# Kernel optimization log

Measured on AMD Instinct MI355X. Metric: run time of the kernel, lower is better.

The kernel has to match this reference:

```python
import jax, jax.numpy as jnp
import numpy as np

INPUT_SIZE = 1024
HIDDEN_SIZE = 1024
LN_EPS = 1e-5


def setup_inputs() -> dict:
    key = jax.random.key(0)
    ks = jax.random.split(key, 8)
    bs, n = 4, 2048
    # Xavier-uniform bound for square (in=out) linear layers
    bound = float(np.sqrt(6.0 / (INPUT_SIZE + HIDDEN_SIZE)))
    x = jax.random.normal(ks[0], (bs, n, INPUT_SIZE), dtype=jnp.float32)
    wq = jax.random.uniform(ks[1], (INPUT_SIZE, HIDDEN_SIZE), jnp.float32, -bound, bound)
    wk = jax.random.uniform(ks[2], (INPUT_SIZE, HIDDEN_SIZE), jnp.float32, -bound, bound)
    wv = jax.random.uniform(ks[3], (INPUT_SIZE, HIDDEN_SIZE), jnp.float32, -bound, bound)
    bq = jnp.zeros((HIDDEN_SIZE,), jnp.float32)
    bk = jnp.zeros((HIDDEN_SIZE,), jnp.float32)
    bv = jnp.zeros((HIDDEN_SIZE,), jnp.float32)
    ln_w = jnp.ones((INPUT_SIZE,), jnp.float32)
    ln_b = jnp.zeros((INPUT_SIZE,), jnp.float32)
    return {"x": x, "wq": wq, "bq": bq, "wk": wk, "bk": bk,
            "wv": wv, "bv": bv, "ln_w": ln_w, "ln_b": ln_b}


def _layernorm(x, w, b):
    mu = jnp.mean(x, axis=-1, keepdims=True)
    var = jnp.mean(jnp.square(x - mu), axis=-1, keepdims=True)
    return (x - mu) * jax.lax.rsqrt(var + LN_EPS) * w + b


def reference(x, wq, bq, wk, bk, wv, bv, ln_w, ln_b):
    # x: [b, n, d_in]
    xn = _layernorm(x, ln_w, ln_b)
    q = jnp.einsum('bnd,dh->bnh', xn, wq) + bq
    k = jnp.einsum('bnd,dh->bnh', xn, wk) + bk
    v = jnp.einsum('bnd,dh->bnh', xn, wv) + bv
    scale = 1.0 / np.sqrt(HIDDEN_SIZE)
    att = jnp.einsum('bqh,bkh->bqk', q, k) * scale  # [b, n, n]
    att = jax.nn.softmax(att, axis=-1)
    out = jnp.einsum('bqk,bkh->bqh', att, v)  # [b, n, h]
    return (att, out)
```

## Files before the change

### kernel.cpp

```cpp
#include <hip/hip_runtime.h>
#include <stdint.h>


typedef __attribute__((ext_vector_type(8))) short short8;
typedef __attribute__((ext_vector_type(4))) float floatx4;
typedef __attribute__((ext_vector_type(4))) uint16_t u16x4;

__device__ __forceinline__ uint16_t f2bf(float f) {
    union { float f; uint32_t u; } v; v.f = f;
    uint32_t r = v.u + 0x7fffu + ((v.u >> 16) & 1u);
    return (uint16_t)(r >> 16);
}

typedef const uint32_t __attribute__((address_space(1)))* gas1_t;
typedef uint32_t __attribute__((address_space(3)))* las3_t;
__device__ __forceinline__ void gload_lds16(const uint16_t* g, uint16_t* l) {
    __builtin_amdgcn_global_load_lds((gas1_t)g, (las3_t)l, 16, 0, 0);
}

__device__ __forceinline__ void s_bar()  { asm volatile("s_barrier" ::: "memory"); }
__device__ __forceinline__ void lgkm0()  { asm volatile("s_waitcnt lgkmcnt(0)" ::: "memory"); }
template<int N> __device__ __forceinline__ void vmw() {
    asm volatile("s_waitcnt vmcnt(%0)" :: "n"(N) : "memory");
}


#define RA(MF, MI)                                                        \
    { Af[(MF)][0] = *(const short8*)(LA + aoff + (MI) * 1024 + ksg0);     \
      Af[(MF)][1] = *(const short8*)(LA + aoff + (MI) * 1024 + ksg1); }
#define RB(NI)                                                            \
    { Bf[(NI)][0] = *(const short8*)(LB + boff + (NI) * 1024 + ksg0);     \
      Bf[(NI)][1] = *(const short8*)(LB + boff + (NI) * 1024 + ksg1); }
#define CLUST(MA, MF, NI0)                                                \
    __builtin_amdgcn_s_setprio(1);                                        \
    _Pragma("unroll") for (int mi = 0; mi < 4; ++mi)                      \
    _Pragma("unroll") for (int nn = 0; nn < 2; ++nn)                      \
    _Pragma("unroll") for (int ks = 0; ks < 2; ++ks)                      \
        acc[(MA) + mi][(NI0) + nn] =                                      \
            __builtin_amdgcn_mfma_f32_16x16x32_bf16(                      \
                Af[(MF) + mi][ks], Bf[(NI0) + nn][ks],                    \
                acc[(MA) + mi][(NI0) + nn], 0, 0, 0);                     \
    __builtin_amdgcn_s_setprio(0);
#define CLUST1(NI)                                                        \
    __builtin_amdgcn_s_setprio(1);                                        \
    _Pragma("unroll") for (int mi = 0; mi < 8; ++mi)                      \
    _Pragma("unroll") for (int ks = 0; ks < 2; ++ks)                      \
        acc[mi][(NI)] = __builtin_amdgcn_mfma_f32_16x16x32_bf16(          \
            Af[mi][ks], Bf[(NI)][ks], acc[mi][(NI)], 0, 0, 0);            \
    __builtin_amdgcn_s_setprio(0);

template<int BN, int EPI>
__device__ __forceinline__ void gemm_core(
    const uint16_t* __restrict__ A, const uint16_t* __restrict__ Bt,
    const int K, const int NT, const int m0, const int n0,
    float* __restrict__ Cf, uint16_t* __restrict__ Cb, const int ldc,
    const float* __restrict__ bq, const float* __restrict__ bk,
    const float* __restrict__ bv, const float alpha)
{
    constexpr int ABUF  = 256 * 64;
    constexpr int BP    = BN / 64;
    constexpr int BBUF  = BN * 64;
    constexpr int BUFSZ = ABUF + BBUF;
    constexpr int OPS   = 4 + BP;
    constexpr int NBUF  = (BN == 128) ? 3 : 2;
    constexpr int WAVES_N = (BN == 128) ? 2 : 4;
    constexpr int MIW  = (BN == 128) ? 4 : 8;
    constexpr int NIW  = BN / (16 * WAVES_N);
    constexpr int NFR  = (BN == 256) ? 4 : MIW;
    __shared__ uint16_t sm[NBUF * BUFSZ + 4096];
    uint16_t* const trash = sm + NBUF * BUFSZ;

    const int t = threadIdx.x;

    const int srow = t >> 3;
    const int sseg = (t & 7) ^ (srow & 7);
    const uint16_t* gA = A + (size_t)(m0 + srow) * K + sseg * 8;
    const uint16_t* gB = Bt + (size_t)(n0 + srow) * K + sseg * 8;

    auto STGALL = [&](int kt, int bi) {
        const int live = kt < NT;
        const size_t ko = (size_t)(live ? kt : 0) * 64;
        uint16_t* const db = sm + bi * BUFSZ + t * 8;
        uint16_t* const tr = trash + t * 8;
#pragma unroll
        for (int p = 0; p < 4; ++p)
            gload_lds16(gA + (size_t)(p * 64) * K + ko,
                        live ? (db + p * 4096) : tr);
#pragma unroll
        for (int p = 0; p < BP; ++p)
            gload_lds16(gB + (size_t)(p * 64) * K + ko,
                        live ? (db + ABUF + p * 4096) : tr);
    };

    const int lane = t & 63;
    const int wid  = t >> 6;
    const int wm   = wid / WAVES_N;
    const int wn   = wid % WAVES_N;
    const int quad = lane >> 4;
    const int lrow = lane & 15;
    const int swz  = lrow & 7;
    const int ksg0 = (quad ^ swz) * 8;
    const int ksg1 = ((4 + quad) ^ swz) * 8;
    const int aoff = (wm * (16 * MIW) + lrow) * 64;
    const int boff = (wn * (16 * NIW) + lrow) * 64;

    floatx4 acc[MIW][NIW];
#pragma unroll
    for (int mi = 0; mi < MIW; ++mi)
#pragma unroll
        for (int ni = 0; ni < NIW; ++ni)
            acc[mi][ni] = floatx4{0.f, 0.f, 0.f, 0.f};

    short8 Af[NFR][2];
    short8 Bf[NIW][2];

    STGALL(0, 0);
    STGALL(1, 1);
    vmw<OPS>();
    s_bar();

    int bcur = 0, bstage = 2;
    for (int te = 0; te < NT; ++te) {
        const int bi = (BN == 128) ? bcur : (te & 1);
        const uint16_t* LA = sm + bi * BUFSZ;
        const uint16_t* LB = LA + ABUF;

        if constexpr (BN == 256) {
            RA(0, 0) RA(1, 1) RA(2, 2) RA(3, 3)
            RB(0) RB(1) RB(2) RB(3)
            CLUST(0, 0, 0) CLUST(0, 0, 2)
            RA(0, 4) RA(1, 5) RA(2, 6) RA(3, 7)
            lgkm0(); s_bar();
            STGALL(te + 2, bi);
            CLUST(4, 0, 0) CLUST(4, 0, 2)
            vmw<OPS>(); s_bar();
        } else if constexpr (BN == 192) {
            RA(0, 0) RA(1, 1) RA(2, 2) RA(3, 3)
            RA(4, 4) RA(5, 5) RA(6, 6) RA(7, 7)
            RB(0) RB(1) RB(2)
            CLUST(0, 0, 0) CLUST(4, 4, 0)
            lgkm0(); s_bar();
            STGALL(te + 2, bi);
            CLUST1(2)
            vmw<OPS>(); s_bar();
        } else {
            STGALL(te + 2, bstage);
            RA(0, 0) RA(1, 1) RA(2, 2) RA(3, 3)
            RB(0) RB(1) RB(2) RB(3)
            CLUST(0, 0, 0) CLUST(0, 0, 2)
            lgkm0();
            vmw<OPS>(); s_bar();
            bcur   = (bcur == 2) ? 0 : bcur + 1;
            bstage = (bstage == 2) ? 0 : bstage + 1;
        }
    }

    vmw<0>();

    const int rbase = m0 + wm * (16 * MIW) + quad * 4;
    const int cbase = n0 + wn * (16 * NIW) + lrow;

    if constexpr (EPI == 1) {
        float bc[NIW];
#pragma unroll
        for (int ni = 0; ni < NIW; ++ni) {
            const int col = cbase + ni * 16;
            const int z = col >> 10;
            const float* bp = (z == 0) ? bq : ((z == 1) ? bk : bv);
            bc[ni] = bp[col & 1023];
        }
#pragma unroll
        for (int mi = 0; mi < MIW; ++mi) {
#pragma unroll
            for (int ni = 0; ni < NIW; ++ni) {
                const int row = rbase + mi * 16;
                const int col = cbase + ni * 16;
                const int z = col >> 10, h = col & 1023;
#pragma unroll
                for (int r = 0; r < 4; ++r)
                    Cb[(size_t)z * 8388608 + (size_t)(row + r) * 1024 + h] =
                        f2bf(acc[mi][ni][r] + bc[ni]);
            }
        }
    } else {
#pragma unroll
        for (int mi = 0; mi < MIW; ++mi) {
#pragma unroll
            for (int ni = 0; ni < NIW; ++ni) {
                const int row = rbase + mi * 16;
                const int col = cbase + ni * 16;
#pragma unroll
                for (int r = 0; r < 4; ++r)
                    Cf[(size_t)(row + r) * ldc + col] = acc[mi][ni][r] * alpha;
            }
        }
    }
}

__global__ __launch_bounds__(512, 2) void k_qkv(
    const uint16_t* __restrict__ xn, const uint16_t* __restrict__ wt,
    const float* __restrict__ bq, const float* __restrict__ bk,
    const float* __restrict__ bv, uint16_t* __restrict__ qkv)
{
    const int flat = blockIdx.y * 16 + blockIdx.x;
    const int s = (flat & 7) * 64 + (flat >> 3);
    const int bx = s & 15, by = s >> 4;
    gemm_core<192, 1>(xn, wt, 1024, 16, by * 256, bx * 192,
                      nullptr, qkv, 0, bq, bk, bv, 0.f);
}

__global__ __launch_bounds__(512, 2) void k_scores(
    const uint16_t* __restrict__ q, const uint16_t* __restrict__ k,
    float* __restrict__ S)
{
    const int flat = blockIdx.z * 64 + blockIdx.y * 8 + blockIdx.x;
    const int s = (flat & 7) * 32 + (flat >> 3);
    const int z = s >> 6, y = (s >> 3) & 7, x = s & 7;
    gemm_core<256, 0>(q + (size_t)z * 2048 * 1024, k + (size_t)z * 2048 * 1024,
                      1024, 16, y * 256, x * 256,
                      S + (size_t)z * 2048 * 2048, nullptr, 2048,
                      nullptr, nullptr, nullptr, 0.03125f);
}

__global__ __launch_bounds__(512, 2) void k_out(
    const uint16_t* __restrict__ attb, const uint16_t* __restrict__ vt,
    float* __restrict__ out)
{
    const int flat = blockIdx.z * 64 + blockIdx.y * 8 + blockIdx.x;
    const int s = (flat & 7) * 32 + (flat >> 3);
    const int z = s >> 6, y = (s >> 3) & 7, x = s & 7;
    gemm_core<128, 0>(attb + (size_t)z * 2048 * 2048, vt + (size_t)z * 1024 * 2048,
                      2048, 32, y * 256, x * 128,
                      out + (size_t)z * 2048 * 1024, nullptr, 1024,
                      nullptr, nullptr, nullptr, 1.0f);
}

__global__ __launch_bounds__(256) void k_ln(
    const float* __restrict__ x, const float* __restrict__ lw,
    const float* __restrict__ lb, uint16_t* __restrict__ xn)
{
    const int row = blockIdx.x;
    const int t = threadIdx.x;
    const float* xr = x + (size_t)row * 1024;
    const float4 xv = ((const float4*)xr)[t];
    float s  = xv.x + xv.y + xv.z + xv.w;
    float s2 = xv.x * xv.x + xv.y * xv.y + xv.z * xv.z + xv.w * xv.w;
#pragma unroll
    for (int off = 32; off > 0; off >>= 1) {
        s  += __shfl_xor(s, off);
        s2 += __shfl_xor(s2, off);
    }
    __shared__ float ps[4], ps2[4];
    const int w = t >> 6, lane = t & 63;
    if (lane == 0) { ps[w] = s; ps2[w] = s2; }
    __syncthreads();
    s  = ps[0] + ps[1] + ps[2] + ps[3];
    s2 = ps2[0] + ps2[1] + ps2[2] + ps2[3];
    const float mu  = s * (1.f / 1024.f);
    const float var = s2 * (1.f / 1024.f) - mu * mu;
    const float rs  = rsqrtf(var + 1e-5f);
    const float4 wv = ((const float4*)lw)[t];
    const float4 bv = ((const float4*)lb)[t];
    u16x4 o;
    o.x = f2bf((xv.x - mu) * rs * wv.x + bv.x);
    o.y = f2bf((xv.y - mu) * rs * wv.y + bv.y);
    o.z = f2bf((xv.z - mu) * rs * wv.z + bv.z);
    o.w = f2bf((xv.w - mu) * rs * wv.w + bv.w);
    ((u16x4*)(xn + (size_t)row * 1024))[t] = o;
}

__global__ void k_wt(const float* __restrict__ wq, const float* __restrict__ wk,
                     const float* __restrict__ wv, uint16_t* __restrict__ wt)
{
    __shared__ float tile[32][33];
    const int z = blockIdx.z;
    const float* W = (z == 0) ? wq : ((z == 1) ? wk : wv);
    uint16_t* T = wt + (size_t)z * 1024 * 1024;
    const int c0 = blockIdx.x * 32, r0 = blockIdx.y * 32;
    const int tx = threadIdx.x, ty = threadIdx.y;
#pragma unroll
    for (int i = 0; i < 4; i++)
        tile[ty + 8 * i][tx] = W[(size_t)(r0 + ty + 8 * i) * 1024 + c0 + tx];
    __syncthreads();
#pragma unroll
    for (int i = 0; i < 4; i++)
        T[(size_t)(c0 + ty + 8 * i) * 1024 + r0 + tx] = f2bf(tile[tx][ty + 8 * i]);
}

__global__ __launch_bounds__(256) void k_vt(
    const uint16_t* __restrict__ v, uint16_t* __restrict__ vt)
{
    __shared__ uint16_t tile[64][68];
    const int b = blockIdx.z;
    const uint16_t* V = v + (size_t)b * 2048 * 1024;
    uint16_t* T = vt + (size_t)b * 1024 * 2048;
    const int h0 = blockIdx.x * 64, t0 = blockIdx.y * 64;
    const int t = threadIdx.x;
    const int rr = t >> 4;
    const int cc = (t & 15) * 4;
#pragma unroll
    for (int i = 0; i < 4; i++) {
        const int tok = rr + 16 * i;
        *(u16x4*)&tile[tok][cc] =
            *(const u16x4*)&V[(size_t)(t0 + tok) * 1024 + h0 + cc];
    }
    __syncthreads();
#pragma unroll
    for (int i = 0; i < 4; i++) {
        const int h = rr + 16 * i;
        u16x4 o;
        o.x = tile[cc + 0][h];
        o.y = tile[cc + 1][h];
        o.z = tile[cc + 2][h];
        o.w = tile[cc + 3][h];
        *(u16x4*)&T[(size_t)(h0 + h) * 2048 + t0 + cc] = o;
    }
}

__global__ __launch_bounds__(256) void k_softmax(
    float* __restrict__ S, uint16_t* __restrict__ attb)
{
    const size_t row = blockIdx.x;
    float* p = S + row * 2048;
    const int t = threadIdx.x;
    float4 a = ((float4*)p)[2 * t];
    float4 b = ((float4*)p)[2 * t + 1];
    float m = fmaxf(fmaxf(fmaxf(a.x, a.y), fmaxf(a.z, a.w)),
                    fmaxf(fmaxf(b.x, b.y), fmaxf(b.z, b.w)));
#pragma unroll
    for (int off = 32; off > 0; off >>= 1) m = fmaxf(m, __shfl_xor(m, off));
    __shared__ float pm[4], pl[4];
    const int w = t >> 6, lane = t & 63;
    if (lane == 0) pm[w] = m;
    __syncthreads();
    m = fmaxf(fmaxf(pm[0], pm[1]), fmaxf(pm[2], pm[3]));

    a.x = __expf(a.x - m); a.y = __expf(a.y - m);
    a.z = __expf(a.z - m); a.w = __expf(a.w - m);
    b.x = __expf(b.x - m); b.y = __expf(b.y - m);
    b.z = __expf(b.z - m); b.w = __expf(b.w - m);
    float s = a.x + a.y + a.z + a.w + b.x + b.y + b.z + b.w;
#pragma unroll
    for (int off = 32; off > 0; off >>= 1) s += __shfl_xor(s, off);
    if (lane == 0) pl[w] = s;
    __syncthreads();
    s = pl[0] + pl[1] + pl[2] + pl[3];
    const float inv = 1.f / s;

    a.x *= inv; a.y *= inv; a.z *= inv; a.w *= inv;
    b.x *= inv; b.y *= inv; b.z *= inv; b.w *= inv;
    ((float4*)p)[2 * t]     = a;
    ((float4*)p)[2 * t + 1] = b;

    uint16_t* q = attb + row * 2048 + t * 8;
    u16x4 o0, o1;
    o0.x = f2bf(a.x); o0.y = f2bf(a.y); o0.z = f2bf(a.z); o0.w = f2bf(a.w);
    o1.x = f2bf(b.x); o1.y = f2bf(b.y); o1.z = f2bf(b.z); o1.w = f2bf(b.w);
    ((u16x4*)q)[0] = o0;
    ((u16x4*)q)[1] = o1;
}

extern "C" void kernel_launch(void* const* d_in, const int* in_sizes, int n_in,
                              void* d_out, int out_size, void* d_ws, size_t ws_size,
                              hipStream_t stream)
{
    const float* x  = (const float*)d_in[0];
    const float* wq = (const float*)d_in[1];
    const float* bq = (const float*)d_in[2];
    const float* wk = (const float*)d_in[3];
    const float* bk = (const float*)d_in[4];
    const float* wv = (const float*)d_in[5];
    const float* bv = (const float*)d_in[6];
    const float* lw = (const float*)d_in[7];
    const float* lb = (const float*)d_in[8];

    float* att = (float*)d_out;
    float* out = (float*)d_out + (size_t)16777216;

    uint16_t* xn = (uint16_t*)d_out;
    uint16_t* wt = (uint16_t*)d_out + (size_t)8388608;

    uint16_t* ws   = (uint16_t*)d_ws;
    uint16_t* q    = ws;
    uint16_t* k    = ws + (size_t)8388608;
    uint16_t* v    = ws + (size_t)2 * 8388608;
    uint16_t* vt   = ws;
    uint16_t* attb = ws + (size_t)8388608;
    uint16_t* qkv  = q;

    if (ws_size < (size_t)50331648) return;

    k_ln<<<8192, 256, 0, stream>>>(x, lw, lb, xn);
    k_wt<<<dim3(32, 32, 3), dim3(32, 8), 0, stream>>>(wq, wk, wv, wt);
    k_qkv<<<dim3(16, 32), 512, 0, stream>>>(xn, wt, bq, bk, bv, qkv);
    k_scores<<<dim3(8, 8, 4), 512, 0, stream>>>(q, k, att);
    k_vt<<<dim3(16, 32, 4), 256, 0, stream>>>(v, vt);
    k_softmax<<<8192, 256, 0, stream>>>(att, attb);
    k_out<<<dim3(8, 8, 4), 512, 0, stream>>>(attb, vt, out);
}
```

Before: 307.3 us.

## Software-pipeline LDS fragment reads across k-halves and retile scores GEMM to 256x128

```diff
diff --git a/kernel.cpp b/kernel.cpp
--- a/kernel.cpp
+++ b/kernel.cpp
@@ -25,28 +25,21 @@
 }
 
 
-#define RA(MF, MI)                                                        \
-    { Af[(MF)][0] = *(const short8*)(LA + aoff + (MI) * 1024 + ksg0);     \
-      Af[(MF)][1] = *(const short8*)(LA + aoff + (MI) * 1024 + ksg1); }
-#define RB(NI)                                                            \
-    { Bf[(NI)][0] = *(const short8*)(LB + boff + (NI) * 1024 + ksg0);     \
-      Bf[(NI)][1] = *(const short8*)(LB + boff + (NI) * 1024 + ksg1); }
-#define CLUST(MA, MF, NI0)                                                \
+#define READS(BASE, KS)                                                   \
+    { const uint16_t* LBp = (BASE) + ABUF;                                \
+      _Pragma("unroll") for (int mi = 0; mi < MIW; ++mi)                  \
+          Af[mi][KS] = *(const short8*)((BASE) + aoff + mi * 1024 +       \
+                                        ((KS) ? ksg1 : ksg0));            \
+      _Pragma("unroll") for (int ni = 0; ni < NIW; ++ni)                  \
+          Bf[ni][KS] = *(const short8*)(LBp + boff + ni * 1024 +          \
+                                        ((KS) ? ksg1 : ksg0)); }
+
+#define MFMAS(KS)                                                         \
     __builtin_amdgcn_s_setprio(1);                                        \
-    _Pragma("unroll") for (int mi = 0; mi < 4; ++mi)                      \
-    _Pragma("unroll") for (int nn = 0; nn < 2; ++nn)                      \
-    _Pragma("unroll") for (int ks = 0; ks < 2; ++ks)                      \
-        acc[(MA) + mi][(NI0) + nn] =                                      \
-            __builtin_amdgcn_mfma_f32_16x16x32_bf16(                      \
-                Af[(MF) + mi][ks], Bf[(NI0) + nn][ks],                    \
-                acc[(MA) + mi][(NI0) + nn], 0, 0, 0);                     \
-    __builtin_amdgcn_s_setprio(0);
-#define CLUST1(NI)                                                        \
-    __builtin_amdgcn_s_setprio(1);                                        \
-    _Pragma("unroll") for (int mi = 0; mi < 8; ++mi)                      \
-    _Pragma("unroll") for (int ks = 0; ks < 2; ++ks)                      \
-        acc[mi][(NI)] = __builtin_amdgcn_mfma_f32_16x16x32_bf16(          \
-            Af[mi][ks], Bf[(NI)][ks], acc[mi][(NI)], 0, 0, 0);            \
+    _Pragma("unroll") for (int mi = 0; mi < MIW; ++mi)                    \
+    _Pragma("unroll") for (int ni = 0; ni < NIW; ++ni)                    \
+        acc[mi][ni] = __builtin_amdgcn_mfma_f32_16x16x32_bf16(            \
+            Af[mi][KS], Bf[ni][KS], acc[mi][ni], 0, 0, 0);                \
     __builtin_amdgcn_s_setprio(0);
 
 template<int BN, int EPI>
@@ -66,7 +59,6 @@
     constexpr int WAVES_N = (BN == 128) ? 2 : 4;
     constexpr int MIW  = (BN == 128) ? 4 : 8;
     constexpr int NIW  = BN / (16 * WAVES_N);
-    constexpr int NFR  = (BN == 256) ? 4 : MIW;
     __shared__ uint16_t sm[NBUF * BUFSZ + 4096];
     uint16_t* const trash = sm + NBUF * BUFSZ;
 
@@ -111,45 +103,42 @@
         for (int ni = 0; ni < NIW; ++ni)
             acc[mi][ni] = floatx4{0.f, 0.f, 0.f, 0.f};
 
-    short8 Af[NFR][2];
+    short8 Af[MIW][2];
     short8 Bf[NIW][2];
 
     STGALL(0, 0);
     STGALL(1, 1);
     vmw<OPS>();
     s_bar();
+    READS(sm, 0);
 
     int bcur = 0, bstage = 2;
     for (int te = 0; te < NT; ++te) {
-        const int bi = (BN == 128) ? bcur : (te & 1);
-        const uint16_t* LA = sm + bi * BUFSZ;
-        const uint16_t* LB = LA + ABUF;
-
-        if constexpr (BN == 256) {
-            RA(0, 0) RA(1, 1) RA(2, 2) RA(3, 3)
-            RB(0) RB(1) RB(2) RB(3)
-            CLUST(0, 0, 0) CLUST(0, 0, 2)
-            RA(0, 4) RA(1, 5) RA(2, 6) RA(3, 7)
-            lgkm0(); s_bar();
-            STGALL(te + 2, bi);
-            CLUST(4, 0, 0) CLUST(4, 0, 2)
-            vmw<OPS>(); s_bar();
-        } else if constexpr (BN == 192) {
-            RA(0, 0) RA(1, 1) RA(2, 2) RA(3, 3)
-            RA(4, 4) RA(5, 5) RA(6, 6) RA(7, 7)
-            RB(0) RB(1) RB(2)
-            CLUST(0, 0, 0) CLUST(4, 4, 0)
-            lgkm0(); s_bar();
-            STGALL(te + 2, bi);
-            CLUST1(2)
-            vmw<OPS>(); s_bar();
+        const uint16_t* LA;
+        const uint16_t* LAn;
+        if constexpr (BN == 128) {
+            LA = sm + bcur * BUFSZ;
+            const int bnext = (bcur == 2) ? 0 : bcur + 1;
+            LAn = sm + bnext * BUFSZ;
+            STGALL(te + 2, bstage);
         } else {
-            STGALL(te + 2, bstage);
-            RA(0, 0) RA(1, 1) RA(2, 2) RA(3, 3)
-            RB(0) RB(1) RB(2) RB(3)
-            CLUST(0, 0, 0) CLUST(0, 0, 2)
-            lgkm0();
-            vmw<OPS>(); s_bar();
+            LA  = sm + (te & 1) * BUFSZ;
+            LAn = sm + ((te + 1) & 1) * BUFSZ;
+        }
+
+        READS(LA, 1);
+        MFMAS(0);
+        lgkm0();
+        if constexpr (BN != 128) {
+            s_bar();
+            STGALL(te + 2, te & 1);
+        }
+        vmw<OPS>();
+        s_bar();
+        READS(LAn, 0);
+        MFMAS(1);
+
+        if constexpr (BN == 128) {
             bcur   = (bcur == 2) ? 0 : bcur + 1;
             bstage = (bstage == 2) ? 0 : bstage + 1;
         }
@@ -213,11 +202,11 @@
     const uint16_t* __restrict__ q, const uint16_t* __restrict__ k,
     float* __restrict__ S)
 {
-    const int flat = blockIdx.z * 64 + blockIdx.y * 8 + blockIdx.x;
-    const int s = (flat & 7) * 32 + (flat >> 3);
-    const int z = s >> 6, y = (s >> 3) & 7, x = s & 7;
-    gemm_core<256, 0>(q + (size_t)z * 2048 * 1024, k + (size_t)z * 2048 * 1024,
-                      1024, 16, y * 256, x * 256,
+    const int flat = (blockIdx.z * 8 + blockIdx.y) * 16 + blockIdx.x;
+    const int s = (flat & 7) * 64 + (flat >> 3);
+    const int x = s & 15, y = (s >> 4) & 7, z = s >> 7;
+    gemm_core<128, 0>(q + (size_t)z * 2048 * 1024, k + (size_t)z * 2048 * 1024,
+                      1024, 16, y * 256, x * 128,
                       S + (size_t)z * 2048 * 2048, nullptr, 2048,
                       nullptr, nullptr, nullptr, 0.03125f);
 }
@@ -393,7 +382,7 @@
     k_ln<<<8192, 256, 0, stream>>>(x, lw, lb, xn);
     k_wt<<<dim3(32, 32, 3), dim3(32, 8), 0, stream>>>(wq, wk, wv, wt);
     k_qkv<<<dim3(16, 32), 512, 0, stream>>>(xn, wt, bq, bk, bv, qkv);
-    k_scores<<<dim3(8, 8, 4), 512, 0, stream>>>(q, k, att);
+    k_scores<<<dim3(16, 8, 4), 512, 0, stream>>>(q, k, att);
     k_vt<<<dim3(16, 32, 4), 256, 0, stream>>>(v, vt);
     k_softmax<<<8192, 256, 0, stream>>>(att, attb);
     k_out<<<dim3(8, 8, 4), 512, 0, stream>>>(attb, vt, out);
```

Result: no change. 306.7 us (-0.2%).

## Restructure GEMM mainloop into 8-phase ping-pong with split staged loads

Applied to the files above, without the earlier changes.

```diff
diff --git a/kernel.cpp b/kernel.cpp
--- a/kernel.cpp
+++ b/kernel.cpp
@@ -25,12 +25,12 @@
 }
 
 
-#define RA(MF, MI)                                                        \
-    { Af[(MF)][0] = *(const short8*)(LA + aoff + (MI) * 1024 + ksg0);     \
-      Af[(MF)][1] = *(const short8*)(LA + aoff + (MI) * 1024 + ksg1); }
-#define RB(NI)                                                            \
-    { Bf[(NI)][0] = *(const short8*)(LB + boff + (NI) * 1024 + ksg0);     \
-      Bf[(NI)][1] = *(const short8*)(LB + boff + (NI) * 1024 + ksg1); }
+#define RA(P, MF, MI)                                                     \
+    { Af[(MF)][0] = *(const short8*)((P) + aoff + (MI) * 1024 + ksg0);    \
+      Af[(MF)][1] = *(const short8*)((P) + aoff + (MI) * 1024 + ksg1); }
+#define RB(P, NI)                                                         \
+    { Bf[(NI)][0] = *(const short8*)((P) + ABUF + boff + (NI) * 1024 + ksg0); \
+      Bf[(NI)][1] = *(const short8*)((P) + ABUF + boff + (NI) * 1024 + ksg1); }
 #define CLUST(MA, MF, NI0)                                                \
     __builtin_amdgcn_s_setprio(1);                                        \
     _Pragma("unroll") for (int mi = 0; mi < 4; ++mi)                      \
@@ -48,27 +48,28 @@
         acc[mi][(NI)] = __builtin_amdgcn_mfma_f32_16x16x32_bf16(          \
             Af[mi][ks], Bf[(NI)][ks], acc[mi][(NI)], 0, 0, 0);            \
     __builtin_amdgcn_s_setprio(0);
+#define PH_MID() s_bar(); lgkm0(); __builtin_amdgcn_sched_barrier(0)
 
 template<int BN, int EPI>
-__device__ __forceinline__ void gemm_core(
+__device__ __forceinline__ void gemm8p(
     const uint16_t* __restrict__ A, const uint16_t* __restrict__ Bt,
     const int K, const int NT, const int m0, const int n0,
     float* __restrict__ Cf, uint16_t* __restrict__ Cb, const int ldc,
     const float* __restrict__ bq, const float* __restrict__ bk,
     const float* __restrict__ bv, const float alpha)
 {
-    constexpr int ABUF  = 256 * 64;
-    constexpr int BP    = BN / 64;
+    constexpr int ABUF  = 16384;
     constexpr int BBUF  = BN * 64;
     constexpr int BUFSZ = ABUF + BBUF;
-    constexpr int OPS   = 4 + BP;
-    constexpr int NBUF  = (BN == 128) ? 3 : 2;
-    constexpr int WAVES_N = (BN == 128) ? 2 : 4;
-    constexpr int MIW  = (BN == 128) ? 4 : 8;
-    constexpr int NIW  = BN / (16 * WAVES_N);
-    constexpr int NFR  = (BN == 256) ? 4 : MIW;
-    __shared__ uint16_t sm[NBUF * BUFSZ + 4096];
-    uint16_t* const trash = sm + NBUF * BUFSZ;
+    constexpr int WN    = (BN == 128) ? 2 : 4;
+    constexpr int WM    = 8 / WN;
+    constexpr int MIW   = 256 / (16 * WM);
+    constexpr int NIW   = BN / (16 * WN);
+    constexpr int NFRA  = (BN == 256) ? 4 : MIW;
+    __shared__ uint16_t sm[2 * BUFSZ + 4096];
+    uint16_t* const trash = sm + 2 * BUFSZ;
+    const uint16_t* const E = sm;
+    const uint16_t* const O = sm + BUFSZ;
 
     const int t = threadIdx.x;
 
@@ -77,25 +78,31 @@
     const uint16_t* gA = A + (size_t)(m0 + srow) * K + sseg * 8;
     const uint16_t* gB = Bt + (size_t)(n0 + srow) * K + sseg * 8;
 
-    auto STGALL = [&](int kt, int bi) {
-        const int live = kt < NT;
-        const size_t ko = (size_t)(live ? kt : 0) * 64;
-        uint16_t* const db = sm + bi * BUFSZ + t * 8;
-        uint16_t* const tr = trash + t * 8;
-#pragma unroll
-        for (int p = 0; p < 4; ++p)
-            gload_lds16(gA + (size_t)(p * 64) * K + ko,
-                        live ? (db + p * 4096) : tr);
-#pragma unroll
-        for (int p = 0; p < BP; ++p)
-            gload_lds16(gB + (size_t)(p * 64) * K + ko,
-                        live ? (db + ABUF + p * 4096) : tr);
+    auto STGA = [&](int kt, int b, int h) {
+        const bool lv = kt < NT;
+        const size_t ko = (size_t)(lv ? kt : 0) * 64;
+        uint16_t* d0 = lv ? (sm + b * BUFSZ + h * 8192 + t * 8) : (trash + t * 8);
+        uint16_t* d1 = lv ? (sm + b * BUFSZ + h * 8192 + 4096 + t * 8) : (trash + t * 8);
+        gload_lds16(gA + (size_t)(h * 128) * K + ko, d0);
+        gload_lds16(gA + (size_t)(h * 128 + 64) * K + ko, d1);
+    };
+    auto STGB = [&](int kt, int b, int u0, int nu) {
+        const bool lv = kt < NT;
+        const size_t ko = (size_t)(lv ? kt : 0) * 64;
+#pragma unroll
+        for (int p = 0; p < 4; ++p) {
+            if (p < nu) {
+                uint16_t* d = lv ? (sm + b * BUFSZ + ABUF + (u0 + p) * 4096 + t * 8)
+                                 : (trash + t * 8);
+                gload_lds16(gB + (size_t)((u0 + p) * 64) * K + ko, d);
+            }
+        }
     };
 
     const int lane = t & 63;
     const int wid  = t >> 6;
-    const int wm   = wid / WAVES_N;
-    const int wn   = wid % WAVES_N;
+    const int wm   = wid / WN;
+    const int wn   = wid % WN;
     const int quad = lane >> 4;
     const int lrow = lane & 15;
     const int swz  = lrow & 7;
@@ -111,47 +118,74 @@
         for (int ni = 0; ni < NIW; ++ni)
             acc[mi][ni] = floatx4{0.f, 0.f, 0.f, 0.f};
 
-    short8 Af[NFR][2];
+    short8 Af[NFRA][2];
     short8 Bf[NIW][2];
 
-    STGALL(0, 0);
-    STGALL(1, 1);
-    vmw<OPS>();
-    s_bar();
-
-    int bcur = 0, bstage = 2;
-    for (int te = 0; te < NT; ++te) {
-        const int bi = (BN == 128) ? bcur : (te & 1);
-        const uint16_t* LA = sm + bi * BUFSZ;
-        const uint16_t* LB = LA + ABUF;
-
-        if constexpr (BN == 256) {
-            RA(0, 0) RA(1, 1) RA(2, 2) RA(3, 3)
-            RB(0) RB(1) RB(2) RB(3)
-            CLUST(0, 0, 0) CLUST(0, 0, 2)
-            RA(0, 4) RA(1, 5) RA(2, 6) RA(3, 7)
-            lgkm0(); s_bar();
-            STGALL(te + 2, bi);
-            CLUST(4, 0, 0) CLUST(4, 0, 2)
-            vmw<OPS>(); s_bar();
-        } else if constexpr (BN == 192) {
-            RA(0, 0) RA(1, 1) RA(2, 2) RA(3, 3)
-            RA(4, 4) RA(5, 5) RA(6, 6) RA(7, 7)
-            RB(0) RB(1) RB(2)
-            CLUST(0, 0, 0) CLUST(4, 4, 0)
-            lgkm0(); s_bar();
-            STGALL(te + 2, bi);
-            CLUST1(2)
-            vmw<OPS>(); s_bar();
-        } else {
-            STGALL(te + 2, bstage);
-            RA(0, 0) RA(1, 1) RA(2, 2) RA(3, 3)
-            RB(0) RB(1) RB(2) RB(3)
-            CLUST(0, 0, 0) CLUST(0, 0, 2)
-            lgkm0();
-            vmw<OPS>(); s_bar();
-            bcur   = (bcur == 2) ? 0 : bcur + 1;
-            bstage = (bstage == 2) ? 0 : bstage + 1;
+    if constexpr (BN == 256) {
+        STGB(0, 0, 0, 2); STGA(0, 0, 0); STGB(0, 0, 2, 2); STGA(0, 0, 1);
+        STGB(1, 1, 0, 2); STGA(1, 1, 0); STGB(1, 1, 2, 2);
+        vmw<6>(); s_bar();
+        for (int te = 0; te < NT; te += 2) {
+            STGA(te + 1, 1, 1);
+            RA(E, 0, 0) RA(E, 1, 1) RA(E, 2, 2) RA(E, 3, 3) RB(E, 0) RB(E, 1)
+            PH_MID(); CLUST(0, 0, 0); s_bar();
+            RB(E, 2) RB(E, 3)
+            PH_MID(); CLUST(0, 0, 2); s_bar();
+            STGB(te + 2, 0, 0, 2);
+            RA(E, 0, 4) RA(E, 1, 5) RA(E, 2, 6) RA(E, 3, 7)
+            PH_MID(); CLUST(4, 0, 0); s_bar();
+            STGA(te + 2, 0, 0); STGB(te + 2, 0, 2, 2);
+            PH_MID(); CLUST(4, 0, 2); vmw<6>(); s_bar();
+            STGA(te + 2, 0, 1);
+            RA(O, 0, 0) RA(O, 1, 1) RA(O, 2, 2) RA(O, 3, 3) RB(O, 0) RB(O, 1)
+            PH_MID(); CLUST(0, 0, 0); s_bar();
+            RB(O, 2) RB(O, 3)
+            PH_MID(); CLUST(0, 0, 2); s_bar();
+            STGB(te + 3, 1, 0, 2);
+            RA(O, 0, 4) RA(O, 1, 5) RA(O, 2, 6) RA(O, 3, 7)
+            PH_MID(); CLUST(4, 0, 0); s_bar();
+            STGA(te + 3, 1, 0); STGB(te + 3, 1, 2, 2);
+            PH_MID(); CLUST(4, 0, 2); vmw<6>(); s_bar();
+        }
+    } else if constexpr (BN == 192) {
+        STGA(0, 0, 0); STGA(0, 0, 1); STGB(0, 0, 0, 3);
+        STGA(1, 1, 0); STGA(1, 1, 1);
+        vmw<4>(); s_bar();
+        for (int te = 0; te < NT; te += 2) {
+            STGB(te + 1, 1, 0, 3);
+            RA(E, 0, 0) RA(E, 1, 1) RA(E, 2, 2) RA(E, 3, 3) RB(E, 0) RB(E, 1)
+            PH_MID(); CLUST(0, 0, 0); s_bar();
+            RA(E, 4, 4) RA(E, 5, 5) RA(E, 6, 6) RA(E, 7, 7)
+            PH_MID(); CLUST(4, 4, 0); s_bar();
+            STGA(te + 2, 0, 0); STGA(te + 2, 0, 1);
+            RB(E, 2)
+            PH_MID(); CLUST1(2); vmw<4>(); s_bar();
+            STGB(te + 2, 0, 0, 3);
+            RA(O, 0, 0) RA(O, 1, 1) RA(O, 2, 2) RA(O, 3, 3) RB(O, 0) RB(O, 1)
+            PH_MID(); CLUST(0, 0, 0); s_bar();
+            RA(O, 4, 4) RA(O, 5, 5) RA(O, 6, 6) RA(O, 7, 7)
+            PH_MID(); CLUST(4, 4, 0); s_bar();
+            STGA(te + 3, 1, 0); STGA(te + 3, 1, 1);
+            RB(O, 2)
+            PH_MID(); CLUST1(2); vmw<4>(); s_bar();
+        }
+    } else {
+        STGA(0, 0, 0); STGA(0, 0, 1); STGB(0, 0, 0, 2);
+        STGA(1, 1, 0); STGA(1, 1, 1);
+        vmw<4>(); s_bar();
+        for (int te = 0; te < NT; te += 2) {
+            STGB(te + 1, 1, 0, 2);
+            RA(E, 0, 0) RA(E, 1, 1) RA(E, 2, 2) RA(E, 3, 3) RB(E, 0) RB(E, 1)
+            PH_MID(); CLUST(0, 0, 0); s_bar();
+            STGA(te + 2, 0, 0); STGA(te + 2, 0, 1);
+            RB(E, 2) RB(E, 3)
+            PH_MID(); CLUST(0, 0, 2); vmw<4>(); s_bar();
+            STGB(te + 2, 0, 0, 2);
+            RA(O, 0, 0) RA(O, 1, 1) RA(O, 2, 2) RA(O, 3, 3) RB(O, 0) RB(O, 1)
+            PH_MID(); CLUST(0, 0, 0); s_bar();
+            STGA(te + 3, 1, 0); STGA(te + 3, 1, 1);
+            RB(O, 2) RB(O, 3)
+            PH_MID(); CLUST(0, 0, 2); vmw<4>(); s_bar();
         }
     }
 
@@ -205,8 +239,8 @@
     const int flat = blockIdx.y * 16 + blockIdx.x;
     const int s = (flat & 7) * 64 + (flat >> 3);
     const int bx = s & 15, by = s >> 4;
-    gemm_core<192, 1>(xn, wt, 1024, 16, by * 256, bx * 192,
-                      nullptr, qkv, 0, bq, bk, bv, 0.f);
+    gemm8p<192, 1>(xn, wt, 1024, 16, by * 256, bx * 192,
+                   nullptr, qkv, 0, bq, bk, bv, 0.f);
 }
 
 __global__ __launch_bounds__(512, 2) void k_scores(
@@ -216,10 +250,10 @@
     const int flat = blockIdx.z * 64 + blockIdx.y * 8 + blockIdx.x;
     const int s = (flat & 7) * 32 + (flat >> 3);
     const int z = s >> 6, y = (s >> 3) & 7, x = s & 7;
-    gemm_core<256, 0>(q + (size_t)z * 2048 * 1024, k + (size_t)z * 2048 * 1024,
-                      1024, 16, y * 256, x * 256,
-                      S + (size_t)z * 2048 * 2048, nullptr, 2048,
-                      nullptr, nullptr, nullptr, 0.03125f);
+    gemm8p<256, 0>(q + (size_t)z * 2048 * 1024, k + (size_t)z * 2048 * 1024,
+                   1024, 16, y * 256, x * 256,
+                   S + (size_t)z * 2048 * 2048, nullptr, 2048,
+                   nullptr, nullptr, nullptr, 0.03125f);
 }
 
 __global__ __launch_bounds__(512, 2) void k_out(
@@ -229,10 +263,10 @@
     const int flat = blockIdx.z * 64 + blockIdx.y * 8 + blockIdx.x;
     const int s = (flat & 7) * 32 + (flat >> 3);
     const int z = s >> 6, y = (s >> 3) & 7, x = s & 7;
-    gemm_core<128, 0>(attb + (size_t)z * 2048 * 2048, vt + (size_t)z * 1024 * 2048,
-                      2048, 32, y * 256, x * 128,
-                      out + (size_t)z * 2048 * 1024, nullptr, 1024,
-                      nullptr, nullptr, nullptr, 1.0f);
+    gemm8p<128, 0>(attb + (size_t)z * 2048 * 2048, vt + (size_t)z * 1024 * 2048,
+                   2048, 32, y * 256, x * 128,
+                   out + (size_t)z * 2048 * 1024, nullptr, 1024,
+                   nullptr, nullptr, nullptr, 1.0f);
 }
 
 __global__ __launch_bounds__(256) void k_ln(
```

Measured after the change: 310.0 us. No clear change (+0.9%).
